# Optimization experiments

Measured on AMD Instinct MI355X. Metric: run time of the kernel, lower is better.

The kernel has to match this reference:

```python
import jax, jax.numpy as jnp
import numpy as np

THRESHOLD = 0.25
W_CD, W_FID, W_NC, W_SYM, W_DIFF = 1.0, 0.5, 0.1, 0.1, 1.0
KL_BETA = 0.0  # _step = 0 at init -> kl_beta = beta_max * min(1, 0/5000) = 0


def _cdist(p1, p2):
    # torch.cdist(p=2): [B,N,3] x [B,M,3] -> [B,N,M]
    sq1 = jnp.sum(p1 * p1, axis=-1)  # [B,N]
    sq2 = jnp.sum(p2 * p2, axis=-1)  # [B,M]
    d2 = sq1[:, :, None] + sq2[:, None, :] - 2.0 * jnp.einsum('bnd,bmd->bnm', p1, p2)
    return jnp.sqrt(jnp.maximum(d2, 0.0))


def _chamfer_l1(p1, p2):
    dist = _cdist(p1, p2)
    cd = dist.min(axis=2).mean(axis=1) + dist.min(axis=1).mean(axis=1)
    return cd.mean()


def setup_inputs() -> dict:
    key = jax.random.key(0)
    ks = jax.random.split(key, 11)
    B, N, M, P, D = 4, 4096, 4096, 2048, 512
    pn = jax.random.normal(ks[7], (B, 3), dtype=jnp.float32)
    pn = pn / jnp.linalg.norm(pn, axis=-1, keepdims=True)  # unit plane normals
    return {
        'pred': jax.random.normal(ks[0], (B, N, 3), dtype=jnp.float32),
        'full': jax.random.normal(ks[1], (B, M, 3), dtype=jnp.float32),
        'partial': jax.random.normal(ks[2], (B, P, 3), dtype=jnp.float32),
        'mu': jax.random.normal(ks[3], (B, D), dtype=jnp.float32),
        'logvar': jax.random.normal(ks[4], (B, D), dtype=jnp.float32),
        'pred_normals': jax.random.normal(ks[5], (B, N, 3), dtype=jnp.float32),
        'gt_normals': jax.random.normal(ks[6], (B, N, 3), dtype=jnp.float32),
        'plane_normals': pn,
        'plane_offsets': jax.random.normal(ks[8], (B,), dtype=jnp.float32) * 0.1,
        'sym_confidences': jax.random.uniform(ks[9], (B,), dtype=jnp.float32),
        'diffusion_loss': jax.random.uniform(ks[10], (), dtype=jnp.float32),
    }


def reference(pred, full, partial, mu, logvar, pred_normals, gt_normals,
              plane_normals, plane_offsets, sym_confidences, diffusion_loss):
    # chamfer L1
    cd = _chamfer_l1(pred, full)
    # KL divergence of diagonal Gaussian
    kl = (-0.5 * (1.0 + logvar - mu * mu - jnp.exp(logvar))).sum(axis=-1).mean()
    # fidelity: partial -> pred nearest-neighbor distance
    fid = _cdist(partial, pred).min(axis=2).mean()
    # normal consistency: 1 - |cos|
    num = jnp.sum(pred_normals * gt_normals, axis=-1)
    den = jnp.linalg.norm(pred_normals, axis=-1) * jnp.linalg.norm(gt_normals, axis=-1)
    cos = num / jnp.maximum(den, 1e-8)
    nc = (1.0 - jnp.abs(cos)).mean()
    # bilateral symmetry error (confidence-gated), vectorized over batch
    off = jax.lax.stop_gradient(plane_offsets)  # torch uses .item() -> constant
    s = jnp.einsum('bnd,bd->bn', pred, plane_normals) + off[:, None]  # signed dist
    reflected = pred - 2.0 * s[..., None] * plane_normals[:, None, :]
    dist = _cdist(pred, reflected)
    cd_l1_b = dist.min(axis=2).mean(axis=1) + dist.min(axis=1).mean(axis=1)  # [B]
    sym_b = jnp.where(sym_confidences >= THRESHOLD,
                      sym_confidences * cd_l1_b * 0.5, 0.0)
    sym = sym_b.mean()
    total = (W_CD * cd + KL_BETA * kl + W_FID * fid + W_NC * nc
             + W_SYM * sym + W_DIFF * diffusion_loss)
    return total
```

## Files before the change

kernel.cpp:

```cpp
#include <hip/hip_runtime.h>

#define BB 4
#define NN 4096
#define MM 4096
#define PP 2048

#define CPL 32
#define QPB 64
#define QG 4


__global__ __launch_bounds__(128, 2) void fused_kernel(
    const float* __restrict__ pred, const float* __restrict__ full,
    const float* __restrict__ partial, const float* __restrict__ plane_n,
    const float* __restrict__ plane_off,
    const float* __restrict__ pn, const float* __restrict__ gn,
    float* __restrict__ ws)
{
    int blk = blockIdx.x;
    int tid = threadIdx.x;
    __shared__ float wmin[2][QPB];
    __shared__ float sred[2];

    if (blk >= 896) {
        int i = (blk - 896) * 128 + tid;
        const float* p = pn + (size_t)i * 3;
        const float* g = gn + (size_t)i * 3;
        float px = p[0], py = p[1], pz = p[2];
        float gx = g[0], gy = g[1], gz = g[2];
        float num = fmaf(px, gx, fmaf(py, gy, pz * gz));
        float den = sqrtf(fmaf(px, px, fmaf(py, py, pz * pz))) *
                    sqrtf(fmaf(gx, gx, fmaf(gy, gy, gz * gz)));
        float v = 1.f - fabsf(num / fmaxf(den, 1e-8f));
        for (int o = 1; o < 64; o <<= 1) v += __shfl_xor(v, o);
        if ((tid & 63) == 0) sred[tid >> 6] = v;
        __syncthreads();
        if (tid == 0) ws[blk] = sred[0] + sred[1];
        return;
    }

    const float* qptr; const float* cptr; int b, qbase;
    bool reflect = false;
    if (blk < 256) {
        b = blk >> 6; qbase = (blk & 63) * QPB;
        qptr = pred + b * NN * 3; cptr = full + b * MM * 3;
    } else if (blk < 512) {
        int t = blk - 256; b = t >> 6; qbase = (t & 63) * QPB;
        qptr = full + b * MM * 3; cptr = pred + b * NN * 3;
    } else if (blk < 640) {
        int t = blk - 512; b = t >> 5; qbase = (t & 31) * QPB;
        qptr = partial + b * PP * 3; cptr = pred + b * NN * 3;
    } else {
        int t = blk - 640; b = t >> 6; qbase = (t & 63) * QPB;
        qptr = pred + b * NN * 3; cptr = pred + b * NN * 3;
        reflect = true;
    }

    int lane = tid & 63;
    int wv = tid >> 6;
    int cbase = wv * (CPL * 64);

    float nx = 0.f, ny = 0.f, nz = 0.f, noff = 0.f;
    if (reflect) {
        nx = plane_n[b * 3 + 0]; ny = plane_n[b * 3 + 1]; nz = plane_n[b * 3 + 2];
        noff = plane_off[b];
    }

    float cxm2[CPL], cym2[CPL], czm2[CPL], c2[CPL];
#pragma unroll
    for (int k = 0; k < CPL; ++k) {
        const float* cp = cptr + (size_t)(cbase + k * 64 + lane) * 3;
        float x = cp[0], y = cp[1], z = cp[2];
        if (reflect) {
            float sd = fmaf(x, nx, fmaf(y, ny, fmaf(z, nz, noff)));
            float t2 = 2.0f * sd;
            x -= t2 * nx; y -= t2 * ny; z -= t2 * nz;
        }
        c2[k]   = fmaf(x, x, fmaf(y, y, z * z));
        cxm2[k] = -2.f * x; cym2[k] = -2.f * y; czm2[k] = -2.f * z;
    }

    for (int qg = 0; qg < QPB / QG; ++qg) {
        const float* qp = qptr + (size_t)(qbase + qg * QG) * 3;
        float qx[QG], qy[QG], qz[QG], mdv[QG];
#pragma unroll
        for (int j = 0; j < QG; ++j) {
            qx[j] = qp[j * 3 + 0];
            qy[j] = qp[j * 3 + 1];
            qz[j] = qp[j * 3 + 2];
            mdv[j] = 3.4e38f;
        }
#pragma unroll
        for (int k = 0; k < CPL; ++k) {
#pragma unroll
            for (int j = 0; j < QG; ++j) {
                float t = fmaf(czm2[k], qz[j], c2[k]);
                t = fmaf(cym2[k], qy[j], t);
                t = fmaf(cxm2[k], qx[j], t);
                mdv[j] = fminf(mdv[j], t);
            }
        }
#pragma unroll
        for (int j = 0; j < QG; ++j) {
            mdv[j] = fminf(mdv[j], __shfl_xor(mdv[j], 1));
            mdv[j] = fminf(mdv[j], __shfl_xor(mdv[j], 2));
            mdv[j] = fminf(mdv[j], __shfl_xor(mdv[j], 4));
            mdv[j] = fminf(mdv[j], __shfl_xor(mdv[j], 8));
            mdv[j] = fminf(mdv[j], __shfl_xor(mdv[j], 16));
            mdv[j] = fminf(mdv[j], __shfl_xor(mdv[j], 32));
        }
        if (lane == 0) {
#pragma unroll
            for (int j = 0; j < QG; ++j)
                wmin[wv][qg * QG + j] = mdv[j];
        }
    }

    __syncthreads();

    if (tid < QPB) {
        float m = fminf(wmin[0][tid], wmin[1][tid]);
        const float* qp = qptr + (size_t)(qbase + tid) * 3;
        float x = qp[0], y = qp[1], z = qp[2];
        float q2 = fmaf(x, x, fmaf(y, y, z * z));
        float d = sqrtf(fmaxf(q2 + m, 0.f));
        for (int o = 1; o < 64; o <<= 1) d += __shfl_xor(d, o);
        if (tid == 0) ws[blk] = d;
    }
}

__global__ __launch_bounds__(256) void final_kernel(
    const float* __restrict__ ws,
    const float* __restrict__ confs,
    const float* __restrict__ diff,
    float* __restrict__ out)
{
    __shared__ float seg[8];
    int tid = threadIdx.x;
    if (tid < 8) seg[tid] = 0.f;
    __syncthreads();
    for (int i = tid; i < 1024; i += 256) {
        float v = ws[i];
        int sgi;
        if (i < 256) sgi = 0;
        else if (i < 512) sgi = 1;
        else if (i < 640) sgi = 2;
        else if (i < 896) sgi = 3 + ((i - 640) >> 6);
        else sgi = 7;
        atomicAdd(&seg[sgi], v);
    }
    __syncthreads();
    if (tid == 0) {
        const float BN = (float)(BB * NN);
        const float BM = (float)(BB * MM);
        const float BP = (float)(BB * PP);
        float cd  = seg[0] / BN + seg[1] / BM;
        float fid = seg[2] / BP;
        float nc  = seg[7] / BN;
        float sym = 0.f;
#pragma unroll
        for (int b = 0; b < BB; ++b) {
            float conf = confs[b];
            if (conf >= 0.25f) {
                float cdl1 = 2.0f * seg[3 + b] / (float)NN;
                sym += conf * cdl1 * 0.5f;
            }
        }
        sym *= (1.0f / BB);
        out[0] = 1.0f * cd + 0.5f * fid + 0.1f * nc + 0.1f * sym + diff[0];
    }
}

extern "C" void kernel_launch(void* const* d_in, const int* in_sizes, int n_in,
                              void* d_out, int out_size, void* d_ws, size_t ws_size,
                              hipStream_t stream) {
    const float* pred      = (const float*)d_in[0];
    const float* full      = (const float*)d_in[1];
    const float* partial   = (const float*)d_in[2];
    const float* pred_n    = (const float*)d_in[5];
    const float* gt_n      = (const float*)d_in[6];
    const float* plane_n   = (const float*)d_in[7];
    const float* plane_off = (const float*)d_in[8];
    const float* confs     = (const float*)d_in[9];
    const float* diff      = (const float*)d_in[10];
    float* ws = (float*)d_ws;

    fused_kernel<<<1024, 128, 0, stream>>>(pred, full, partial, plane_n,
                                           plane_off, pred_n, gt_n, ws);
    final_kernel<<<1, 256, 0, stream>>>(ws, confs, diff, (float*)d_out);
}
```

Baseline: 41.93 us.

## Precompute packed float4 points and scan broadcast candidates per query lane

A new prep kernel packs pred, full, reflected pred and partial into float4 arrays with squared norms folded in (and -2 scaling for query sides). The nearest-neighbor kernel then maps one query per lane and streams wave-uniform candidate float4s, which can become scalar loads. This removes the per-query cross-lane shuffle min-reduction and the in-kernel reflection recomputation, and it moves to 256-thread blocks with 4 candidate splits. The cost is an extra kernel launch plus a workspace round trip, and the hot loop now depends on scalar-memory throughput.

Measured after the change: 127.5 us. 3.04x slower.

```diff
diff --git a/kernel.cpp b/kernel.cpp
--- a/kernel.cpp
+++ b/kernel.cpp
@@ -2,28 +2,61 @@
 
 #define BB 4
 #define NN 4096
-#define MM 4096
 #define PP 2048
+#define CSPLIT 1024
 
-#define CPL 32
-#define QPB 64
-#define QG 4
+#define RAWFULL 0
+#define RAWPRED 16384
+#define RAWREFL 32768
+#define SQPRED  49152
+#define SQFULL  65536
+#define SQPART  81920
+
+__global__ __launch_bounds__(256) void prep_kernel(
+    const float* __restrict__ pred, const float* __restrict__ full,
+    const float* __restrict__ partial, const float* __restrict__ plane_n,
+    const float* __restrict__ plane_off, float4* __restrict__ a4)
+{
+    int i = blockIdx.x * 256 + threadIdx.x;
+    int b = i >> 12, j = i & 4095;
+    const float* f = full + (size_t)i * 3;
+    float x = f[0], y = f[1], z = f[2];
+    float s2 = fmaf(x, x, fmaf(y, y, z * z));
+    a4[RAWFULL + i] = make_float4(x, y, z, s2);
+    a4[SQFULL + i]  = make_float4(-2.f * x, -2.f * y, -2.f * z, s2);
+    const float* p = pred + (size_t)i * 3;
+    float px = p[0], py = p[1], pz = p[2];
+    float p2 = fmaf(px, px, fmaf(py, py, pz * pz));
+    a4[RAWPRED + i] = make_float4(px, py, pz, p2);
+    a4[SQPRED + i]  = make_float4(-2.f * px, -2.f * py, -2.f * pz, p2);
+    float nx = plane_n[b * 3], ny = plane_n[b * 3 + 1], nz = plane_n[b * 3 + 2];
+    float off = plane_off[b];
+    float sd = fmaf(px, nx, fmaf(py, ny, fmaf(pz, nz, off)));
+    float rx = px - 2.f * sd * nx, ry = py - 2.f * sd * ny, rz = pz - 2.f * sd * nz;
+    float r2 = fmaf(rx, rx, fmaf(ry, ry, rz * rz));
+    a4[RAWREFL + i] = make_float4(rx, ry, rz, r2);
+    if (j < PP) {
+        int pi = b * PP + j;
+        const float* q = partial + (size_t)pi * 3;
+        float qx = q[0], qy = q[1], qz = q[2];
+        float q2 = fmaf(qx, qx, fmaf(qy, qy, qz * qz));
+        a4[SQPART + pi] = make_float4(-2.f * qx, -2.f * qy, -2.f * qz, q2);
+    }
+}
 
 
-__global__ __launch_bounds__(128, 2) void fused_kernel(
-    const float* __restrict__ pred, const float* __restrict__ full,
-    const float* __restrict__ partial, const float* __restrict__ plane_n,
-    const float* __restrict__ plane_off,
+__global__ __launch_bounds__(256) void nn_kernel(
+    const float4* __restrict__ a4,
     const float* __restrict__ pn, const float* __restrict__ gn,
-    float* __restrict__ ws)
+    float* __restrict__ res)
 {
     int blk = blockIdx.x;
     int tid = threadIdx.x;
-    __shared__ float wmin[2][QPB];
-    __shared__ float sred[2];
+    __shared__ float wmin[4][64];
+    __shared__ float sred[4];
 
     if (blk >= 896) {
-        int i = (blk - 896) * 128 + tid;
+        int i = (blk - 896) * 256 + tid;
         const float* p = pn + (size_t)i * 3;
         const float* g = gn + (size_t)i * 3;
         float px = p[0], py = p[1], pz = p[2];
@@ -35,102 +68,57 @@
         for (int o = 1; o < 64; o <<= 1) v += __shfl_xor(v, o);
         if ((tid & 63) == 0) sred[tid >> 6] = v;
         __syncthreads();
-        if (tid == 0) ws[blk] = sred[0] + sred[1];
+        if (tid == 0) res[blk] = sred[0] + sred[1] + sred[2] + sred[3];
         return;
     }
 
-    const float* qptr; const float* cptr; int b, qbase;
-    bool reflect = false;
+    int qoff, coff;
     if (blk < 256) {
-        b = blk >> 6; qbase = (blk & 63) * QPB;
-        qptr = pred + b * NN * 3; cptr = full + b * MM * 3;
+        int b = blk >> 6; qoff = SQPRED + b * 4096 + (blk & 63) * 64;
+        coff = RAWFULL + b * 4096;
     } else if (blk < 512) {
-        int t = blk - 256; b = t >> 6; qbase = (t & 63) * QPB;
-        qptr = full + b * MM * 3; cptr = pred + b * NN * 3;
+        int t = blk - 256; int b = t >> 6;
+        qoff = SQFULL + b * 4096 + (t & 63) * 64;
+        coff = RAWPRED + b * 4096;
     } else if (blk < 640) {
-        int t = blk - 512; b = t >> 5; qbase = (t & 31) * QPB;
-        qptr = partial + b * PP * 3; cptr = pred + b * NN * 3;
+        int t = blk - 512; int b = t >> 5;
+        qoff = SQPART + b * 2048 + (t & 31) * 64;
+        coff = RAWPRED + b * 4096;
     } else {
-        int t = blk - 640; b = t >> 6; qbase = (t & 63) * QPB;
-        qptr = pred + b * NN * 3; cptr = pred + b * NN * 3;
-        reflect = true;
+        int t = blk - 640; int b = t >> 6;
+        qoff = SQPRED + b * 4096 + (t & 63) * 64;
+        coff = RAWREFL + b * 4096;
     }
 
     int lane = tid & 63;
-    int wv = tid >> 6;
-    int cbase = wv * (CPL * 64);
+    int wv = __builtin_amdgcn_readfirstlane(tid >> 6);
 
-    float nx = 0.f, ny = 0.f, nz = 0.f, noff = 0.f;
-    if (reflect) {
-        nx = plane_n[b * 3 + 0]; ny = plane_n[b * 3 + 1]; nz = plane_n[b * 3 + 2];
-        noff = plane_off[b];
+    float4 q = a4[qoff + lane];
+    const float4* __restrict__ cp = a4 + coff + wv * CSPLIT;
+
+    float md = 3.4e38f;
+#pragma unroll 8
+    for (int k = 0; k < CSPLIT; k += 2) {
+        float4 ca = cp[k];
+        float4 cb = cp[k + 1];
+        float ta = fmaf(ca.x, q.x, fmaf(ca.y, q.y, fmaf(ca.z, q.z, ca.w)));
+        float tb = fmaf(cb.x, q.x, fmaf(cb.y, q.y, fmaf(cb.z, q.z, cb.w)));
+        md = fminf(md, fminf(ta, tb));
     }
-
-    float cxm2[CPL], cym2[CPL], czm2[CPL], c2[CPL];
-#pragma unroll
-    for (int k = 0; k < CPL; ++k) {
-        const float* cp = cptr + (size_t)(cbase + k * 64 + lane) * 3;
-        float x = cp[0], y = cp[1], z = cp[2];
-        if (reflect) {
-            float sd = fmaf(x, nx, fmaf(y, ny, fmaf(z, nz, noff)));
-            float t2 = 2.0f * sd;
-            x -= t2 * nx; y -= t2 * ny; z -= t2 * nz;
-        }
-        c2[k]   = fmaf(x, x, fmaf(y, y, z * z));
-        cxm2[k] = -2.f * x; cym2[k] = -2.f * y; czm2[k] = -2.f * z;
-    }
-
-    for (int qg = 0; qg < QPB / QG; ++qg) {
-        const float* qp = qptr + (size_t)(qbase + qg * QG) * 3;
-        float qx[QG], qy[QG], qz[QG], mdv[QG];
-#pragma unroll
-        for (int j = 0; j < QG; ++j) {
-            qx[j] = qp[j * 3 + 0];
-            qy[j] = qp[j * 3 + 1];
-            qz[j] = qp[j * 3 + 2];
-            mdv[j] = 3.4e38f;
-        }
-#pragma unroll
-        for (int k = 0; k < CPL; ++k) {
-#pragma unroll
-            for (int j = 0; j < QG; ++j) {
-                float t = fmaf(czm2[k], qz[j], c2[k]);
-                t = fmaf(cym2[k], qy[j], t);
-                t = fmaf(cxm2[k], qx[j], t);
-                mdv[j] = fminf(mdv[j], t);
-            }
-        }
-#pragma unroll
-        for (int j = 0; j < QG; ++j) {
-            mdv[j] = fminf(mdv[j], __shfl_xor(mdv[j], 1));
-            mdv[j] = fminf(mdv[j], __shfl_xor(mdv[j], 2));
-            mdv[j] = fminf(mdv[j], __shfl_xor(mdv[j], 4));
-            mdv[j] = fminf(mdv[j], __shfl_xor(mdv[j], 8));
-            mdv[j] = fminf(mdv[j], __shfl_xor(mdv[j], 16));
-            mdv[j] = fminf(mdv[j], __shfl_xor(mdv[j], 32));
-        }
-        if (lane == 0) {
-#pragma unroll
-            for (int j = 0; j < QG; ++j)
-                wmin[wv][qg * QG + j] = mdv[j];
-        }
-    }
-
+    wmin[wv][lane] = md;
     __syncthreads();
 
-    if (tid < QPB) {
-        float m = fminf(wmin[0][tid], wmin[1][tid]);
-        const float* qp = qptr + (size_t)(qbase + tid) * 3;
-        float x = qp[0], y = qp[1], z = qp[2];
-        float q2 = fmaf(x, x, fmaf(y, y, z * z));
-        float d = sqrtf(fmaxf(q2 + m, 0.f));
+    if (tid < 64) {
+        float m = fminf(fminf(wmin[0][tid], wmin[1][tid]),
+                        fminf(wmin[2][tid], wmin[3][tid]));
+        float d = sqrtf(fmaxf(q.w + m, 0.f));
         for (int o = 1; o < 64; o <<= 1) d += __shfl_xor(d, o);
-        if (tid == 0) ws[blk] = d;
+        if (tid == 0) res[blk] = d;
     }
 }
 
 __global__ __launch_bounds__(256) void final_kernel(
-    const float* __restrict__ ws,
+    const float* __restrict__ res,
     const float* __restrict__ confs,
     const float* __restrict__ diff,
     float* __restrict__ out)
@@ -139,8 +127,8 @@
     int tid = threadIdx.x;
     if (tid < 8) seg[tid] = 0.f;
     __syncthreads();
-    for (int i = tid; i < 1024; i += 256) {
-        float v = ws[i];
+    for (int i = tid; i < 960; i += 256) {
+        float v = res[i];
         int sgi;
         if (i < 256) sgi = 0;
         else if (i < 512) sgi = 1;
@@ -152,9 +140,8 @@
     __syncthreads();
     if (tid == 0) {
         const float BN = (float)(BB * NN);
-        const float BM = (float)(BB * MM);
         const float BP = (float)(BB * PP);
-        float cd  = seg[0] / BN + seg[1] / BM;
+        float cd  = seg[0] / BN + seg[1] / BN;
         float fid = seg[2] / BP;
         float nc  = seg[7] / BN;
         float sym = 0.f;
@@ -184,8 +171,10 @@
     const float* confs     = (const float*)d_in[9];
     const float* diff      = (const float*)d_in[10];
     float* ws = (float*)d_ws;
+    float4* a4 = (float4*)(ws + 4096);
 
-    fused_kernel<<<1024, 128, 0, stream>>>(pred, full, partial, plane_n,
-                                           plane_off, pred_n, gt_n, ws);
+    prep_kernel<<<64, 256, 0, stream>>>(pred, full, partial, plane_n,
+                                        plane_off, a4);
+    nn_kernel<<<960, 256, 0, stream>>>(a4, pred_n, gt_n, ws);
     final_kernel<<<1, 256, 0, stream>>>(ws, confs, diff, (float*)d_out);
 }
```
